# Kernel optimization log

Measured on AMD Instinct MI355X. Metric: run time of the kernel, lower is better.

The kernel has to match this reference:

```python
import jax, jax.numpy as jnp
import numpy as np

D_MODEL = 1024
NUM_HEADS = 16
THETA = 10000.0


def _rope(x, pos):
    # x: [B, H, S, d_k], pos: [B, S] int
    d = x.shape[-1]
    half = d // 2
    inv_freq = THETA ** (-(jnp.arange(half, dtype=jnp.float32) * 2.0) / d)  # [half]
    ang = pos.astype(jnp.float32)[..., None] * inv_freq                     # [B, S, half]
    cos = jnp.cos(ang)[:, None, :, :]  # [B, 1, S, half]
    sin = jnp.sin(ang)[:, None, :, :]
    x1 = x[..., 0::2]
    x2 = x[..., 1::2]
    r1 = x1 * cos - x2 * sin
    r2 = x1 * sin + x2 * cos
    return jnp.stack([r1, r2], axis=-1).reshape(x.shape)


def setup_inputs() -> dict:
    key = jax.random.key(0)
    ks = jax.random.split(key, 5)
    B, S, D = 2, 2048, D_MODEL
    scale = 1.0 / np.sqrt(D)
    x = jax.random.normal(ks[0], (B, S, D), dtype=jnp.float32)
    token_positions = jnp.broadcast_to(jnp.arange(S, dtype=jnp.int32), (B, S))
    Wq = jax.random.normal(ks[1], (D, D), dtype=jnp.float32) * scale
    Wk = jax.random.normal(ks[2], (D, D), dtype=jnp.float32) * scale
    Wv = jax.random.normal(ks[3], (D, D), dtype=jnp.float32) * scale
    Wo = jax.random.normal(ks[4], (D, D), dtype=jnp.float32) * scale
    return {"x": x, "token_positions": token_positions, "Wq": Wq, "Wk": Wk, "Wv": Wv, "Wo": Wo}


def reference(x, token_positions, Wq, Wk, Wv, Wo):
    B, S, D = x.shape
    H = NUM_HEADS
    dk = D // H
    # Linear: y = x @ W.T (torch nn.Linear convention, no bias)
    q = jnp.einsum('bsd,od->bso', x, Wq).reshape(B, S, H, dk).transpose(0, 2, 1, 3)
    k = jnp.einsum('bsd,od->bso', x, Wk).reshape(B, S, H, dk).transpose(0, 2, 1, 3)
    v = jnp.einsum('bsd,od->bso', x, Wv).reshape(B, S, H, dk).transpose(0, 2, 1, 3)
    q = _rope(q, token_positions)
    k = _rope(k, token_positions)
    scores = jnp.einsum('bhqd,bhkd->bhqk', q, k) / jnp.sqrt(jnp.float32(dk))
    causal = jnp.tril(jnp.ones((S, S), dtype=bool))
    scores = jnp.where(causal, scores, jnp.finfo(scores.dtype).min)
    attn = jax.nn.softmax(scores, axis=-1)
    out = jnp.einsum('bhqk,bhkd->bhqd', attn, v)  # [B, H, S, dk]
    out = out.transpose(0, 2, 1, 3).reshape(B, S, D)
    return jnp.einsum('bsd,od->bso', out, Wo)
```

## Files before the change

kernel.cpp:

```cpp
#include <hip/hip_runtime.h>
#include <stdint.h>

#define S_LEN 2048
#define DMODEL 1024
#define NHEAD 16
#define DK 64
#define BATCH 2

typedef __attribute__((ext_vector_type(8))) short bf16x8;
typedef __attribute__((ext_vector_type(4))) float f32x4;

__device__ __forceinline__ unsigned short f2bf(float f) {
  union { float f; unsigned u; } x; x.f = f;
  unsigned u = x.u;
  return (unsigned short)((u + 0x7fffu + ((u >> 16) & 1u)) >> 16);
}

__device__ __forceinline__ void gload_lds16(const void* g, void* l) {
  __builtin_amdgcn_global_load_lds(
      (const __attribute__((address_space(1))) unsigned int*)g,
      (__attribute__((address_space(3))) unsigned int*)l, 16, 0, 0);
}

__global__ __launch_bounds__(256) void cast_inputs(
    const float4* __restrict__ x,
    const float4* __restrict__ wq, const float4* __restrict__ wk,
    const float4* __restrict__ wv, const float4* __restrict__ wo,
    ushort4* __restrict__ xb, ushort4* __restrict__ wqkvb, ushort4* __restrict__ wob)
{
  int i = blockIdx.x * 256 + threadIdx.x;
  float4 v; ushort4* dst;
  if (i < (1 << 20)) {
    v = x[i]; dst = xb + i;
  } else {
    int j = i - (1 << 20);
    int wsel = j >> 18;
    int o = j & ((1 << 18) - 1);
    const float4* src = (wsel == 0) ? wq : (wsel == 1) ? wk : (wsel == 2) ? wv : wo;
    v = src[o];
    dst = (wsel < 3) ? (wqkvb + ((size_t)wsel << 18) + o) : (wob + o);
  }
  ushort4 r;
  r.x = f2bf(v.x); r.y = f2bf(v.y); r.z = f2bf(v.z); r.w = f2bf(v.w);
  *dst = r;
}

__global__ __launch_bounds__(256) void rope_table(const int* __restrict__ pos,
                                                  float2* __restrict__ rope)
{
  int idx = blockIdx.x * 256 + threadIdx.x;
  int ps = idx >> 5;
  int i = idx & 31;
  float p = (float)pos[ps];
  float freq = exp2f(-(float)i * 0.41524101186092096f);
  float ang = p * freq;
  rope[idx] = make_float2(cosf(ang), sinf(ang));
}

template<int EPI>
__global__ __launch_bounds__(256) void gemm_bt(
    const ushort* __restrict__ A, const ushort* __restrict__ Bw,
    const float2* __restrict__ rope,
    ushort* __restrict__ Qb, ushort* __restrict__ Kb, ushort* __restrict__ Vg,
    float* __restrict__ Out)
{
  constexpr int Kdim = 1024;
  __shared__ ushort At[128 * 64];
  __shared__ ushort Bt[128 * 64];
  const int bm = blockIdx.x & 31;
  const int bn = blockIdx.x >> 5;
  const int tid = threadIdx.x;
  const int w = tid >> 6, lane = tid & 63;
  const int wr = w >> 1, wc = w & 1;
  const int lrow = lane >> 3;
  const int lch = lane & 7;

  f32x4 acc[4][4];
#pragma unroll
  for (int i = 0; i < 4; ++i)
#pragma unroll
    for (int j = 0; j < 4; ++j) acc[i][j] = (f32x4){0.f, 0.f, 0.f, 0.f};

  const size_t abase = (size_t)(bm * 128) * Kdim;
  const size_t bbase = (size_t)(bn * 128) * Kdim;

  for (int kt = 0; kt < Kdim / 64; ++kt) {
#pragma unroll
    for (int inst = 0; inst < 4; ++inst) {
      int r = w * 32 + inst * 8 + lrow;
      int gc = lch ^ (r & 7);
      gload_lds16(A + abase + (size_t)r * Kdim + kt * 64 + gc * 8,
                  &At[(w * 32 + inst * 8) * 64]);
      gload_lds16(Bw + bbase + (size_t)r * Kdim + kt * 64 + gc * 8,
                  &Bt[(w * 32 + inst * 8) * 64]);
    }
    __syncthreads();
    __builtin_amdgcn_s_setprio(1);
#pragma unroll
    for (int kk = 0; kk < 2; ++kk) {
      bf16x8 af[4], bfv[4];
      int ch = kk * 4 + (lane >> 4);
#pragma unroll
      for (int fm = 0; fm < 4; ++fm) {
        int row = wr * 64 + fm * 16 + (lane & 15);
        af[fm] = *(const bf16x8*)&At[row * 64 + ((ch ^ (row & 7)) << 3)];
      }
#pragma unroll
      for (int fn = 0; fn < 4; ++fn) {
        int row = wc * 64 + fn * 16 + (lane & 15);
        bfv[fn] = *(const bf16x8*)&Bt[row * 64 + ((ch ^ (row & 7)) << 3)];
      }
#pragma unroll
      for (int fm = 0; fm < 4; ++fm)
#pragma unroll
        for (int fn = 0; fn < 4; ++fn)
          acc[fm][fn] = __builtin_amdgcn_mfma_f32_16x16x32_bf16(
              af[fm], bfv[fn], acc[fm][fn], 0, 0, 0);
    }
    __builtin_amdgcn_s_setprio(0);
    __syncthreads();
  }

  if constexpr (EPI == 0) {
    const int sel = bn >> 3;
    if (sel == 2) {
#pragma unroll
      for (int fn = 0; fn < 4; ++fn) {
        int gn = bn * 128 + wc * 64 + fn * 16 + (lane & 15);
        int col = gn & 1023;
        int h = col >> 6, d = col & 63;
#pragma unroll
        for (int fm = 0; fm < 4; ++fm) {
          int gm0 = bm * 128 + wr * 64 + fm * 16 + ((lane >> 4) << 2);
          int b = gm0 >> 11, s0 = gm0 & 2047;
          uint lo = (uint)f2bf(acc[fm][fn][0]) | ((uint)f2bf(acc[fm][fn][1]) << 16);
          uint hi = (uint)f2bf(acc[fm][fn][2]) | ((uint)f2bf(acc[fm][fn][3]) << 16);
          uint2 val; val.x = lo; val.y = hi;
          *(uint2*)(Vg + ((size_t)((b * NHEAD + h) * DK + d) * S_LEN) + s0) = val;
        }
      }
    } else {
      ushort* dst0 = (sel == 0) ? Qb : Kb;
#pragma unroll
      for (int fn = 0; fn < 4; ++fn) {
        int gn = bn * 128 + wc * 64 + fn * 16 + (lane & 15);
        int col = gn & 1023;
        int h = col >> 6, d = col & 63;
#pragma unroll
        for (int fm = 0; fm < 4; ++fm) {
          int gm0 = bm * 128 + wr * 64 + fm * 16 + ((lane >> 4) << 2);
#pragma unroll
          for (int j = 0; j < 4; ++j) {
            int gm = gm0 + j;
            float v = acc[fm][fn][j];
            float p = __shfl_xor(v, 1);
            float2 cs = rope[gm * 32 + (d >> 1)];
            float r = (d & 1) ? (v * cs.x + p * cs.y) : (v * cs.x - p * cs.y);
            if (sel == 0) r *= 0.125f;
            int b = gm >> 11, s = gm & 2047;
            dst0[((size_t)(b * NHEAD + h) * S_LEN + s) * DK + d] = f2bf(r);
          }
        }
      }
    }
  } else {
#pragma unroll
    for (int fn = 0; fn < 4; ++fn) {
      int gn = bn * 128 + wc * 64 + fn * 16 + (lane & 15);
#pragma unroll
      for (int fm = 0; fm < 4; ++fm) {
        int gm0 = bm * 128 + wr * 64 + fm * 16 + ((lane >> 4) << 2);
#pragma unroll
        for (int j = 0; j < 4; ++j)
          Out[(size_t)(gm0 + j) * 1024 + gn] = acc[fm][fn][j];
      }
    }
  }
}

__global__ __launch_bounds__(256) void attn_kernel(
    const ushort* __restrict__ Qb, const ushort* __restrict__ Kb,
    const ushort* __restrict__ Vg, ushort* __restrict__ Ob)
{
  __shared__ ushort Kt[2][64 * 64];
  __shared__ ushort Vt[2][64 * 64];
  __shared__ ushort Pt[4][16 * 64];
  const int tid = threadIdx.x;
  const int w = tid >> 6, lane = tid & 63;
  const int g = lane >> 4, q = lane & 15;
  const int bid = blockIdx.x;
  const int swz = (bid & 7) * 64 + (bid >> 3);
  const int bh = swz >> 4, pair = swz & 15;
  const size_t kqbase = (size_t)bh * (S_LEN * DK);
  const size_t vbase  = (size_t)bh * (DK * S_LEN);
  const int b = bh >> 4, h = bh & 15;
  ushort* Pw = Pt[w];
  uint* Pw32 = (uint*)Pw;

  for (int t2 = 0; t2 < 2; ++t2) {
    const int qt = t2 ? (31 - pair) : pair;
    const int qrow0 = qt * 64 + w * 16;

    bf16x8 qf[2];
    {
      const ushort* qp = Qb + kqbase + (size_t)(qrow0 + q) * DK + g * 8;
      qf[0] = *(const bf16x8*)qp;
      qf[1] = *(const bf16x8*)(qp + 32);
    }
    f32x4 oacc[4];
#pragma unroll
    for (int dt = 0; dt < 4; ++dt) oacc[dt] = (f32x4){0.f, 0.f, 0.f, 0.f};
    float m_r = -INFINITY, l_r = 0.f;

#pragma unroll
    for (int pass = 0; pass < 2; ++pass) {
      int r0 = pass * 32 + w * 8;
      int r = r0 + (lane >> 3);
      int gc = (lane & 7) ^ (r & 7);
      gload_lds16(Kb + kqbase + (size_t)r * DK + gc * 8, &Kt[0][r0 * 64]);
      gload_lds16(Vg + vbase + (size_t)r * S_LEN + gc * 8, &Vt[0][r0 * 64]);
    }
    __syncthreads();

    int cur = 0;
    for (int kt = 0; kt <= qt; ++kt) {
      if (kt < qt) {
        int nxt = cur ^ 1, ktn = kt + 1;
#pragma unroll
        for (int pass = 0; pass < 2; ++pass) {
          int r0 = pass * 32 + w * 8;
          int r = r0 + (lane >> 3);
          int gc = (lane & 7) ^ (r & 7);
          gload_lds16(Kb + kqbase + (size_t)(ktn * 64 + r) * DK + gc * 8,
                      &Kt[nxt][r0 * 64]);
          gload_lds16(Vg + vbase + (size_t)r * S_LEN + ktn * 64 + gc * 8,
                      &Vt[nxt][r0 * 64]);
        }
      }

      f32x4 sacc[4];
#pragma unroll
      for (int ct = 0; ct < 4; ++ct) sacc[ct] = (f32x4){0.f, 0.f, 0.f, 0.f};
      __builtin_amdgcn_s_setprio(1);
#pragma unroll
      for (int kk = 0; kk < 2; ++kk) {
        int ch = kk * 4 + g;
#pragma unroll
        for (int ct = 0; ct < 4; ++ct) {
          int row = ct * 16 + q;
          bf16x8 kf = *(const bf16x8*)&Kt[cur][row * 64 + ((ch ^ (row & 7)) << 3)];
          sacc[ct] = __builtin_amdgcn_mfma_f32_16x16x32_bf16(kf, qf[kk], sacc[ct], 0, 0, 0);
        }
      }
      __builtin_amdgcn_s_setprio(0);

      if (kt == qt) {
        int qa = qrow0 + q;
#pragma unroll
        for (int ct = 0; ct < 4; ++ct) {
#pragma unroll
          for (int j = 0; j < 4; ++j) {
            int kv = qt * 64 + ct * 16 + g * 4 + j;
            if (kv > qa) sacc[ct][j] = -INFINITY;
          }
        }
      }

      float mx = sacc[0][0];
#pragma unroll
      for (int ct = 0; ct < 4; ++ct)
#pragma unroll
        for (int j = 0; j < 4; ++j) mx = fmaxf(mx, sacc[ct][j]);
      mx = fmaxf(mx, __shfl_xor(mx, 16));
      mx = fmaxf(mx, __shfl_xor(mx, 32));
      if (mx > m_r + 8.0f) {
        float sc = __expf(m_r - mx);
        m_r = mx;
        l_r *= sc;
#pragma unroll
        for (int dt = 0; dt < 4; ++dt)
#pragma unroll
          for (int j = 0; j < 4; ++j) oacc[dt][j] *= sc;
      }
      float p[4][4];
      float rs = 0.f;
#pragma unroll
      for (int ct = 0; ct < 4; ++ct)
#pragma unroll
        for (int j = 0; j < 4; ++j) {
          float e = __expf(sacc[ct][j] - m_r);
          p[ct][j] = e; rs += e;
        }
      rs += __shfl_xor(rs, 16);
      rs += __shfl_xor(rs, 32);
      l_r += rs;

#pragma unroll
      for (int ct = 0; ct < 4; ++ct)
#pragma unroll
        for (int i = 0; i < 2; ++i) {
          uint u = (uint)f2bf(p[ct][2 * i]) | ((uint)f2bf(p[ct][2 * i + 1]) << 16);
          int idx = 8 * ct + 2 * g + i;
          Pw32[q * 32 + (((idx >> 2) ^ (q & 7)) << 2) + (idx & 3)] = u;
        }
      __builtin_amdgcn_s_setprio(1);
#pragma unroll
      for (int kk = 0; kk < 2; ++kk) {
        int ch = kk * 4 + g;
        bf16x8 pb = *(const bf16x8*)&Pw[q * 64 + ((ch ^ (q & 7)) << 3)];
#pragma unroll
        for (int dt = 0; dt < 4; ++dt) {
          int vr = dt * 16 + q;
          bf16x8 vf = *(const bf16x8*)&Vt[cur][vr * 64 + ((ch ^ (vr & 7)) << 3)];
          oacc[dt] = __builtin_amdgcn_mfma_f32_16x16x32_bf16(vf, pb, oacc[dt], 0, 0, 0);
        }
      }
      __builtin_amdgcn_s_setprio(0);
      __syncthreads();
      cur ^= 1;
    }

    float inv = 1.0f / l_r;
#pragma unroll
    for (int dt = 0; dt < 4; ++dt)
#pragma unroll
      for (int i = 0; i < 2; ++i) {
        uint u = (uint)f2bf(oacc[dt][2 * i] * inv) |
                 ((uint)f2bf(oacc[dt][2 * i + 1] * inv) << 16);
        int idx = dt * 8 + 2 * g + i;
        Pw32[q * 32 + (((idx >> 2) ^ (q & 7)) << 2) + (idx & 3)] = u;
      }
#pragma unroll
    for (int pass = 0; pass < 2; ++pass) {
      int qr = pass * 8 + (lane >> 3), c = lane & 7;
      bf16x8 vv = *(const bf16x8*)&Pw[qr * 64 + ((c ^ (qr & 7)) << 3)];
      *(bf16x8*)(Ob + ((size_t)(b * S_LEN) + qrow0 + qr) * DMODEL + h * DK + c * 8) = vv;
    }
  }
}

extern "C" void kernel_launch(void* const* d_in, const int* in_sizes, int n_in,
                              void* d_out, int out_size, void* d_ws, size_t ws_size,
                              hipStream_t stream) {
  const float* x  = (const float*)d_in[0];
  const int* pos  = (const int*)d_in[1];
  const float* wq = (const float*)d_in[2];
  const float* wk = (const float*)d_in[3];
  const float* wv = (const float*)d_in[4];
  const float* wo = (const float*)d_in[5];
  float* out = (float*)d_out;

  char* ws = (char*)d_ws;
  ushort* xb    = (ushort*)(ws);
  ushort* wqkvb = (ushort*)(ws + (size_t)( 8u << 20));
  ushort* wob   = (ushort*)(ws + (size_t)(14u << 20));
  float2* rope  = (float2*)(ws + (size_t)(16u << 20));
  ushort* Qb    = (ushort*)(ws + (size_t)(17u << 20));
  ushort* Kb    = (ushort*)(ws + (size_t)(25u << 20));
  ushort* Vg    = (ushort*)(ws + (size_t)(33u << 20));
  ushort* Ob    = (ushort*)(ws + (size_t)(41u << 20));

  cast_inputs<<<8192, 256, 0, stream>>>((const float4*)x, (const float4*)wq,
      (const float4*)wk, (const float4*)wv, (const float4*)wo,
      (ushort4*)xb, (ushort4*)wqkvb, (ushort4*)wob);
  rope_table<<<512, 256, 0, stream>>>(pos, rope);
  gemm_bt<0><<<32 * 24, 256, 0, stream>>>(xb, wqkvb, rope, Qb, Kb, Vg, nullptr);
  attn_kernel<<<512, 256, 0, stream>>>(Qb, Kb, Vg, Ob);
  gemm_bt<1><<<32 * 8, 256, 0, stream>>>(Ob, wob, rope, nullptr, nullptr, nullptr, out);
}
```

Baseline: 125.4 us.

## Restructure attention to 32x32 MFMA with register-resident P and exp2 softmax

After: 173.8 us. 38.6% more time.

```diff
diff --git a/kernel.cpp b/kernel.cpp
--- a/kernel.cpp
+++ b/kernel.cpp
@@ -9,6 +9,7 @@
 
 typedef __attribute__((ext_vector_type(8))) short bf16x8;
 typedef __attribute__((ext_vector_type(4))) float f32x4;
+typedef __attribute__((ext_vector_type(16))) float f32x16;
 
 __device__ __forceinline__ unsigned short f2bf(float f) {
   union { float f; unsigned u; } x; x.f = f;
@@ -16,11 +17,19 @@
   return (unsigned short)((u + 0x7fffu + ((u >> 16) & 1u)) >> 16);
 }
 
+__device__ __forceinline__ uint cvt_pk_bf16(float a, float b) {
+  uint r;
+  asm("v_cvt_pk_bf16_f32 %0, %1, %2" : "=v"(r) : "v"(a), "v"(b));
+  return r;
+}
+
 __device__ __forceinline__ void gload_lds16(const void* g, void* l) {
   __builtin_amdgcn_global_load_lds(
       (const __attribute__((address_space(1))) unsigned int*)g,
       (__attribute__((address_space(3))) unsigned int*)l, 16, 0, 0);
 }
+
+#define QSCALE 0.18033688011112042f
 
 __global__ __launch_bounds__(256) void cast_inputs(
     const float4* __restrict__ x,
@@ -134,8 +143,8 @@
           int gm0 = bm * 128 + wr * 64 + fm * 16 + ((lane >> 4) << 2);
           int b = gm0 >> 11, s0 = gm0 & 2047;
           uint lo = (uint)f2bf(acc[fm][fn][0]) | ((uint)f2bf(acc[fm][fn][1]) << 16);
-          uint hi = (uint)f2bf(acc[fm][fn][2]) | ((uint)f2bf(acc[fm][fn][3]) << 16);
-          uint2 val; val.x = lo; val.y = hi;
+          uint hi2 = (uint)f2bf(acc[fm][fn][2]) | ((uint)f2bf(acc[fm][fn][3]) << 16);
+          uint2 val; val.x = lo; val.y = hi2;
           *(uint2*)(Vg + ((size_t)((b * NHEAD + h) * DK + d) * S_LEN) + s0) = val;
         }
       }
@@ -156,7 +165,7 @@
             float p = __shfl_xor(v, 1);
             float2 cs = rope[gm * 32 + (d >> 1)];
             float r = (d & 1) ? (v * cs.x + p * cs.y) : (v * cs.x - p * cs.y);
-            if (sel == 0) r *= 0.125f;
+            if (sel == 0) r *= QSCALE;
             int b = gm >> 11, s = gm & 2047;
             dst0[((size_t)(b * NHEAD + h) * S_LEN + s) * DK + d] = f2bf(r);
           }
@@ -178,165 +187,179 @@
   }
 }
 
-__global__ __launch_bounds__(256) void attn_kernel(
+__global__ __launch_bounds__(128) void attn_kernel(
     const ushort* __restrict__ Qb, const ushort* __restrict__ Kb,
     const ushort* __restrict__ Vg, ushort* __restrict__ Ob)
 {
   __shared__ ushort Kt[2][64 * 64];
   __shared__ ushort Vt[2][64 * 64];
-  __shared__ ushort Pt[4][16 * 64];
   const int tid = threadIdx.x;
   const int w = tid >> 6, lane = tid & 63;
-  const int g = lane >> 4, q = lane & 15;
+  const int hi = lane >> 5, q = lane & 31;
   const int bid = blockIdx.x;
-  const int swz = (bid & 7) * 64 + (bid >> 3);
-  const int bh = swz >> 4, pair = swz & 15;
+  const int gidx = (bid & 7) * 128 + (bid >> 3);
+  const int bh = gidx >> 5;
+  const int qt = 31 - (gidx & 31);
   const size_t kqbase = (size_t)bh * (S_LEN * DK);
   const size_t vbase  = (size_t)bh * (DK * S_LEN);
   const int b = bh >> 4, h = bh & 15;
-  ushort* Pw = Pt[w];
-  uint* Pw32 = (uint*)Pw;
-
-  for (int t2 = 0; t2 < 2; ++t2) {
-    const int qt = t2 ? (31 - pair) : pair;
-    const int qrow0 = qt * 64 + w * 16;
-
-    bf16x8 qf[2];
-    {
-      const ushort* qp = Qb + kqbase + (size_t)(qrow0 + q) * DK + g * 8;
-      qf[0] = *(const bf16x8*)qp;
-      qf[1] = *(const bf16x8*)(qp + 32);
-    }
-    f32x4 oacc[4];
-#pragma unroll
-    for (int dt = 0; dt < 4; ++dt) oacc[dt] = (f32x4){0.f, 0.f, 0.f, 0.f};
-    float m_r = -INFINITY, l_r = 0.f;
-
-#pragma unroll
-    for (int pass = 0; pass < 2; ++pass) {
-      int r0 = pass * 32 + w * 8;
-      int r = r0 + (lane >> 3);
-      int gc = (lane & 7) ^ (r & 7);
-      gload_lds16(Kb + kqbase + (size_t)r * DK + gc * 8, &Kt[0][r0 * 64]);
-      gload_lds16(Vg + vbase + (size_t)r * S_LEN + gc * 8, &Vt[0][r0 * 64]);
+  const int q0w = qt * 64 + w * 32;
+
+  bf16x8 qf[4];
+  {
+    const ushort* qp = Qb + kqbase + (size_t)(q0w + q) * DK + hi * 8;
+#pragma unroll
+    for (int kk = 0; kk < 4; ++kk) qf[kk] = *(const bf16x8*)(qp + kk * 16);
+  }
+  f32x16 oacc[2];
+#pragma unroll
+  for (int dt = 0; dt < 2; ++dt)
+#pragma unroll
+    for (int r = 0; r < 16; ++r) oacc[dt][r] = 0.f;
+  float m_r = -INFINITY, l_r = 0.f;
+
+  const int srow = lane >> 3, sslot = lane & 7;
+
+#define STAGE(buf_, kt_)                                                     \
+  do {                                                                       \
+    _Pragma("unroll") for (int p = 0; p < 4; ++p) {                          \
+      int rr = p * 16 + w * 8 + srow;                                        \
+      int gc = sslot ^ (rr & 7);                                             \
+      gload_lds16(Kb + kqbase + (size_t)((kt_) * 64 + rr) * DK + gc * 8,     \
+                  &Kt[buf_][(p * 16 + w * 8) * 64]);                         \
+      gload_lds16(Vg + vbase + (size_t)rr * S_LEN + (kt_) * 64 + gc * 8,     \
+                  &Vt[buf_][(p * 16 + w * 8) * 64]);                         \
+    }                                                                        \
+  } while (0)
+
+  STAGE(0, 0);
+  __syncthreads();
+  int cur = 0;
+  for (int kt = 0; kt <= qt; ++kt) {
+    if (kt < qt) STAGE(cur ^ 1, kt + 1);
+    const int nct = (kt == qt && w == 0) ? 1 : 2;
+    f32x16 sacc[2];
+#pragma unroll
+    for (int ct = 0; ct < 2; ++ct)
+#pragma unroll
+      for (int r = 0; r < 16; ++r) sacc[ct][r] = 0.f;
+
+    __builtin_amdgcn_s_setprio(1);
+#pragma unroll
+    for (int ct = 0; ct < 2; ++ct) {
+      if (ct < nct) {
+#pragma unroll
+        for (int kk = 0; kk < 4; ++kk) {
+          int row = ct * 32 + q;
+          bf16x8 kf = *(const bf16x8*)
+              &Kt[cur][row * 64 + (((kk * 2 + hi) ^ (row & 7)) << 3)];
+          sacc[ct] = __builtin_amdgcn_mfma_f32_32x32x16_bf16(
+              kf, qf[kk], sacc[ct], 0, 0, 0);
+        }
+      }
+    }
+    __builtin_amdgcn_s_setprio(0);
+
+    if (kt == qt) {
+#pragma unroll
+      for (int r = 0; r < 16; ++r) {
+        int crow = (r & 3) + 8 * (r >> 2) + 4 * hi;
+        bool m = crow > q;
+        if (w == 0) { if (m) sacc[0][r] = -INFINITY; }
+        else        { if (m) sacc[1][r] = -INFINITY; }
+      }
+    }
+
+    float mx = -INFINITY;
+#pragma unroll
+    for (int ct = 0; ct < 2; ++ct)
+      if (ct < nct)
+#pragma unroll
+        for (int r = 0; r < 16; ++r) mx = fmaxf(mx, sacc[ct][r]);
+    mx = fmaxf(mx, __shfl_xor(mx, 32));
+    if (mx > m_r + 8.0f) {
+      float sc = exp2f(m_r - mx);
+      m_r = mx;
+      l_r *= sc;
+#pragma unroll
+      for (int dt = 0; dt < 2; ++dt)
+#pragma unroll
+        for (int r = 0; r < 16; ++r) oacc[dt][r] *= sc;
+    }
+    float rs = 0.f;
+#pragma unroll
+    for (int ct = 0; ct < 2; ++ct)
+      if (ct < nct)
+#pragma unroll
+        for (int r = 0; r < 16; ++r) {
+          float e = exp2f(sacc[ct][r] - m_r);
+          sacc[ct][r] = e;
+          rs += e;
+        }
+    rs += __shfl_xor(rs, 32);
+    l_r += rs;
+
+#pragma unroll
+    for (int ct = 0; ct < 2; ++ct) {
+      if (ct < nct) {
+        uint W8[8], X8[8];
+#pragma unroll
+        for (int r4 = 0; r4 < 4; ++r4)
+#pragma unroll
+          for (int i = 0; i < 2; ++i)
+            W8[r4 * 2 + i] = cvt_pk_bf16(sacc[ct][4 * r4 + 2 * i],
+                                         sacc[ct][4 * r4 + 2 * i + 1]);
+#pragma unroll
+        for (int k = 0; k < 8; ++k) X8[k] = __shfl_xor(W8[k], 32);
+        __builtin_amdgcn_s_setprio(1);
+#pragma unroll
+        for (int kcl = 0; kcl < 2; ++kcl) {
+          int a = 2 * kcl;
+          union { uint u[4]; bf16x8 v; } pb;
+          pb.u[0] = hi ? X8[(a + 1) * 2]     : W8[a * 2];
+          pb.u[1] = hi ? X8[(a + 1) * 2 + 1] : W8[a * 2 + 1];
+          pb.u[2] = hi ? W8[(a + 1) * 2]     : X8[a * 2];
+          pb.u[3] = hi ? W8[(a + 1) * 2 + 1] : X8[a * 2 + 1];
+          int kc2 = ct * 2 + kcl;
+#pragma unroll
+          for (int dt = 0; dt < 2; ++dt) {
+            int row = dt * 32 + q;
+            bf16x8 vf = *(const bf16x8*)
+                &Vt[cur][row * 64 + (((kc2 * 2 + hi) ^ (row & 7)) << 3)];
+            oacc[dt] = __builtin_amdgcn_mfma_f32_32x32x16_bf16(
+                vf, pb.v, oacc[dt], 0, 0, 0);
+          }
+        }
+        __builtin_amdgcn_s_setprio(0);
+      }
     }
     __syncthreads();
-
-    int cur = 0;
-    for (int kt = 0; kt <= qt; ++kt) {
-      if (kt < qt) {
-        int nxt = cur ^ 1, ktn = kt + 1;
-#pragma unroll
-        for (int pass = 0; pass < 2; ++pass) {
-          int r0 = pass * 32 + w * 8;
-          int r = r0 + (lane >> 3);
-          int gc = (lane & 7) ^ (r & 7);
-          gload_lds16(Kb + kqbase + (size_t)(ktn * 64 + r) * DK + gc * 8,
-                      &Kt[nxt][r0 * 64]);
-          gload_lds16(Vg + vbase + (size_t)r * S_LEN + ktn * 64 + gc * 8,
-                      &Vt[nxt][r0 * 64]);
-        }
-      }
-
-      f32x4 sacc[4];
-#pragma unroll
-      for (int ct = 0; ct < 4; ++ct) sacc[ct] = (f32x4){0.f, 0.f, 0.f, 0.f};
-      __builtin_amdgcn_s_setprio(1);
-#pragma unroll
-      for (int kk = 0; kk < 2; ++kk) {
-        int ch = kk * 4 + g;
-#pragma unroll
-        for (int ct = 0; ct < 4; ++ct) {
-          int row = ct * 16 + q;
-          bf16x8 kf = *(const bf16x8*)&Kt[cur][row * 64 + ((ch ^ (row & 7)) << 3)];
-          sacc[ct] = __builtin_amdgcn_mfma_f32_16x16x32_bf16(kf, qf[kk], sacc[ct], 0, 0, 0);
-        }
-      }
-      __builtin_amdgcn_s_setprio(0);
-
-      if (kt == qt) {
-        int qa = qrow0 + q;
-#pragma unroll
-        for (int ct = 0; ct < 4; ++ct) {
-#pragma unroll
-          for (int j = 0; j < 4; ++j) {
-            int kv = qt * 64 + ct * 16 + g * 4 + j;
-            if (kv > qa) sacc[ct][j] = -INFINITY;
-          }
-        }
-      }
-
-      float mx = sacc[0][0];
-#pragma unroll
-      for (int ct = 0; ct < 4; ++ct)
-#pragma unroll
-        for (int j = 0; j < 4; ++j) mx = fmaxf(mx, sacc[ct][j]);
-      mx = fmaxf(mx, __shfl_xor(mx, 16));
-      mx = fmaxf(mx, __shfl_xor(mx, 32));
-      if (mx > m_r + 8.0f) {
-        float sc = __expf(m_r - mx);
-        m_r = mx;
-        l_r *= sc;
-#pragma unroll
-        for (int dt = 0; dt < 4; ++dt)
-#pragma unroll
-          for (int j = 0; j < 4; ++j) oacc[dt][j] *= sc;
-      }
-      float p[4][4];
-      float rs = 0.f;
-#pragma unroll
-      for (int ct = 0; ct < 4; ++ct)
-#pragma unroll
-        for (int j = 0; j < 4; ++j) {
-          float e = __expf(sacc[ct][j] - m_r);
-          p[ct][j] = e; rs += e;
-        }
-      rs += __shfl_xor(rs, 16);
-      rs += __shfl_xor(rs, 32);
-      l_r += rs;
-
-#pragma unroll
-      for (int ct = 0; ct < 4; ++ct)
-#pragma unroll
-        for (int i = 0; i < 2; ++i) {
-          uint u = (uint)f2bf(p[ct][2 * i]) | ((uint)f2bf(p[ct][2 * i + 1]) << 16);
-          int idx = 8 * ct + 2 * g + i;
-          Pw32[q * 32 + (((idx >> 2) ^ (q & 7)) << 2) + (idx & 3)] = u;
-        }
-      __builtin_amdgcn_s_setprio(1);
-#pragma unroll
-      for (int kk = 0; kk < 2; ++kk) {
-        int ch = kk * 4 + g;
-        bf16x8 pb = *(const bf16x8*)&Pw[q * 64 + ((ch ^ (q & 7)) << 3)];
-#pragma unroll
-        for (int dt = 0; dt < 4; ++dt) {
-          int vr = dt * 16 + q;
-          bf16x8 vf = *(const bf16x8*)&Vt[cur][vr * 64 + ((ch ^ (vr & 7)) << 3)];
-          oacc[dt] = __builtin_amdgcn_mfma_f32_16x16x32_bf16(vf, pb, oacc[dt], 0, 0, 0);
-        }
-      }
-      __builtin_amdgcn_s_setprio(0);
-      __syncthreads();
-      cur ^= 1;
-    }
-
-    float inv = 1.0f / l_r;
-#pragma unroll
-    for (int dt = 0; dt < 4; ++dt)
+    cur ^= 1;
+  }
+
+  float inv = 1.0f / l_r;
+  uint* Ow = (uint*)&Kt[0][0] + w * 1024;
+#pragma unroll
+  for (int dt = 0; dt < 2; ++dt)
+#pragma unroll
+    for (int r4 = 0; r4 < 4; ++r4)
 #pragma unroll
       for (int i = 0; i < 2; ++i) {
-        uint u = (uint)f2bf(oacc[dt][2 * i] * inv) |
-                 ((uint)f2bf(oacc[dt][2 * i + 1] * inv) << 16);
-        int idx = dt * 8 + 2 * g + i;
-        Pw32[q * 32 + (((idx >> 2) ^ (q & 7)) << 2) + (idx & 3)] = u;
-      }
-#pragma unroll
-    for (int pass = 0; pass < 2; ++pass) {
-      int qr = pass * 8 + (lane >> 3), c = lane & 7;
-      bf16x8 vv = *(const bf16x8*)&Pw[qr * 64 + ((c ^ (qr & 7)) << 3)];
-      *(bf16x8*)(Ob + ((size_t)(b * S_LEN) + qrow0 + qr) * DMODEL + h * DK + c * 8) = vv;
-    }
-  }
+        int wi = dt * 16 + r4 * 4 + hi * 2 + i;
+        uint val = cvt_pk_bf16(oacc[dt][4 * r4 + 2 * i] * inv,
+                               oacc[dt][4 * r4 + 2 * i + 1] * inv);
+        Ow[q * 32 + (((wi >> 2) ^ (q & 7)) << 2) + (wi & 3)] = val;
+      }
+#pragma unroll
+  for (int p = 0; p < 4; ++p) {
+    int idx = p * 64 + lane;
+    int qr = idx >> 3, c = idx & 7;
+    bf16x8 v = *(const bf16x8*)
+        &((const ushort*)Ow)[qr * 64 + ((c ^ (qr & 7)) << 3)];
+    int gq = q0w + qr;
+    *(bf16x8*)(Ob + ((size_t)b * S_LEN + gq) * DMODEL + h * DK + c * 8) = v;
+  }
+#undef STAGE
 }
 
 extern "C" void kernel_launch(void* const* d_in, const int* in_sizes, int n_in,
@@ -365,6 +388,6 @@
       (ushort4*)xb, (ushort4*)wqkvb, (ushort4*)wob);
   rope_table<<<512, 256, 0, stream>>>(pos, rope);
   gemm_bt<0><<<32 * 24, 256, 0, stream>>>(xb, wqkvb, rope, Qb, Kb, Vg, nullptr);
-  attn_kernel<<<512, 256, 0, stream>>>(Qb, Kb, Vg, Ob);
+  attn_kernel<<<1024, 128, 0, stream>>>(Qb, Kb, Vg, Ob);
   gemm_bt<1><<<32 * 8, 256, 0, stream>>>(Ob, wob, rope, nullptr, nullptr, nullptr, out);
 }
```
